# Performance work log

Hardware: AMD Instinct MI355X
Metric: run time of the kernel (lower is better)

The kernel has to match this reference:

```python
import jax, jax.numpy as jnp
import numpy as np

EPS = 1e-5

def _conv(x, w, stride=1, padding=0):
    return jax.lax.conv_general_dilated(
        x, w, window_strides=(stride, stride),
        padding=((padding, padding), (padding, padding)),
        dimension_numbers=('NCHW', 'OIHW', 'NCHW'))

def _bn(x, gamma, beta, mean, var):
    # inference-mode batchnorm, per-channel over NCHW
    inv = gamma / jnp.sqrt(var + EPS)
    return x * inv[None, :, None, None] + (beta - mean * inv)[None, :, None, None]

def setup_inputs() -> dict:
    key = jax.random.key(0)
    ks = jax.random.split(key, 16)
    B, Cin, H, W = 64, 1024, 28, 28
    width, Cout = 256, 1024
    d = {}
    d['x'] = jax.random.normal(ks[0], (B, Cin, H, W), jnp.float32)
    d['w1'] = jax.random.normal(ks[1], (width, Cin, 1, 1), jnp.float32) * 0.03
    d['w2'] = jax.random.normal(ks[2], (width, width, 3, 3), jnp.float32) * 0.02
    d['w3'] = jax.random.normal(ks[3], (Cout, width, 1, 1), jnp.float32) * 0.03
    for i, c in [(1, width), (2, width), (3, Cout)]:
        d[f'g{i}'] = jnp.ones((c,), jnp.float32)
        d[f'b{i}'] = jnp.zeros((c,), jnp.float32)
        d[f'm{i}'] = jax.random.normal(ks[4 + i], (c,), jnp.float32) * 0.1
        d[f'v{i}'] = jax.random.uniform(ks[8 + i], (c,), jnp.float32, 0.5, 1.5)
    return d

def reference(x, w1, w2, w3, g1, b1, m1, v1, g2, b2, m2, v2, g3, b3, m3, v3):
    out = jax.nn.relu(_bn(_conv(x, w1), g1, b1, m1, v1))
    out = jax.nn.relu(_bn(_conv(out, w2, stride=1, padding=1), g2, b2, m2, v2))
    out = _bn(_conv(out, w3), g3, b3, m3, v3)
    return jax.nn.relu(out + x)
```

## Files before the change

kernel.cpp:

```cpp
#include <hip/hip_runtime.h>
#include <hip/hip_bf16.h>
#include <cstdint>
#include <cstddef>

#define EPS_BN 1e-5f
#define LDK1 40
#define TILE1 (128 * LDK1)

typedef __attribute__((ext_vector_type(8))) __bf16 bf16x8;
typedef __attribute__((ext_vector_type(4))) float f32x4;

__device__ __forceinline__ unsigned short f2b(float f) {
    __hip_bfloat16 h = __float2bfloat16(f);
    return __builtin_bit_cast(unsigned short, h);
}
__device__ __forceinline__ unsigned int pack2(float a, float b) {
    return (unsigned int)f2b(a) | ((unsigned int)f2b(b) << 16);
}
__device__ __forceinline__ void lgkm_barrier() {
    __builtin_amdgcn_s_waitcnt(0xC07F);
    __builtin_amdgcn_s_barrier();
}


__global__ void prep_bn_kernel(const float* __restrict__ g1, const float* __restrict__ b1,
                               const float* __restrict__ m1, const float* __restrict__ v1,
                               const float* __restrict__ g2, const float* __restrict__ b2,
                               const float* __restrict__ m2, const float* __restrict__ v2,
                               const float* __restrict__ g3, const float* __restrict__ b3,
                               const float* __restrict__ m3, const float* __restrict__ v3,
                               float* __restrict__ bias1, float* __restrict__ bias2,
                               float* __restrict__ bias3) {
    int t = blockIdx.x * 256 + threadIdx.x;
    if (t < 256) {
        float inv = g1[t] * rsqrtf(v1[t] + EPS_BN);
        bias1[t] = b1[t] - m1[t] * inv;
    } else if (t < 512) {
        int c = t - 256;
        float inv = g2[c] * rsqrtf(v2[c] + EPS_BN);
        bias2[c] = b2[c] - m2[c] * inv;
    } else if (t < 1536) {
        int c = t - 512;
        float inv = g3[c] * rsqrtf(v3[c] + EPS_BN);
        bias3[c] = b3[c] - m3[c] * inv;
    }
}

__global__ void repack_w1(const float* __restrict__ w1, const float* __restrict__ g1,
                          const float* __restrict__ v1, unsigned short* __restrict__ w1b) {
    int idx = blockIdx.x * 256 + threadIdx.x;
    int co = idx >> 10;
    float inv = g1[co] * rsqrtf(v1[co] + EPS_BN);
    w1b[idx] = f2b(w1[idx] * inv);
}

__global__ void repack_w2(const float* __restrict__ w2, const float* __restrict__ g2,
                          const float* __restrict__ v2, unsigned short* __restrict__ w2r) {
    int idx = blockIdx.x * 256 + threadIdx.x;
    int k9 = idx >> 16;
    int rem = idx & 65535;
    int co = rem >> 8;
    int ci = rem & 255;
    float inv = g2[co] * rsqrtf(v2[co] + EPS_BN);
    w2r[idx] = f2b(w2[(co * 256 + ci) * 9 + k9] * inv);
}

__global__ void repack_w3(const float* __restrict__ w3, const float* __restrict__ g3,
                          const float* __restrict__ v3, unsigned short* __restrict__ w3b) {
    int idx = blockIdx.x * 256 + threadIdx.x;
    int co = idx >> 8;
    float inv = g3[co] * rsqrtf(v3[co] + EPS_BN);
    w3b[idx] = f2b(w3[idx] * inv);
}

__global__ void halo_zero(unsigned short* __restrict__ in2p) {
    int idx = blockIdx.x * 256 + threadIdx.x;
    int cell = idx >> 5, l8 = idx & 31;
    int n = cell / 116, c = cell % 116;
    int h, w;
    if (c < 30)      { h = 0;      w = c; }
    else if (c < 60) { h = 29;     w = c - 30; }
    else if (c < 88) { h = c - 59; w = 0; }
    else             { h = c - 87; w = 29; }
    uint4 z = {0u, 0u, 0u, 0u};
    *reinterpret_cast<uint4*>(in2p + (((size_t)n * 900) + h * 30 + w) * 256 + l8 * 8) = z;
}

__device__ __forceinline__ void mfma_step(const unsigned short* As, const unsigned short* Bs,
                                          int aoff, int boff, int ld, f32x4 acc[4][4]) {
    bf16x8 a[4], b[4];
#pragma unroll
    for (int i = 0; i < 4; ++i)
        a[i] = *reinterpret_cast<const bf16x8*>(As + aoff + i * 16 * ld);
#pragma unroll
    for (int j = 0; j < 4; ++j)
        b[j] = *reinterpret_cast<const bf16x8*>(Bs + boff + j * 16 * ld);
#pragma unroll
    for (int i = 0; i < 4; ++i)
#pragma unroll
        for (int j = 0; j < 4; ++j)
            acc[i][j] = __builtin_amdgcn_mfma_f32_16x16x32_bf16(a[i], b[j], acc[i][j], 0, 0, 0);
}

__global__ __launch_bounds__(512) void conv1_kernel(const float* __restrict__ x,
                                                    const unsigned short* __restrict__ w1b,
                                                    const float* __restrict__ bias1,
                                                    unsigned short* __restrict__ in2p) {
    __shared__ unsigned short As[2][256 * LDK1];
    __shared__ unsigned short Bs[2][128 * LDK1];
    const int tid = threadIdx.x;
    const int f0 = blockIdx.x * 128;
    const int lane = tid & 63, wave = tid >> 6;
    const int wA = wave & 3;
    const int wB = wave >> 2;
    const int l15 = lane & 15, quad = lane >> 4;

    const int ar = tid >> 1, ah = (tid & 1) * 16;
    const unsigned short* aptr = w1b + (size_t)ar * 1024 + ah;
    const int awo = ar * LDK1 + ah;

    const int cp = tid >> 5, sq = tid & 31;
    const float* xb[4];
    int bwo[4];
#pragma unroll
    for (int e = 0; e < 4; ++e) {
        int f = f0 + sq + 32 * e;
        int n = f / 784, sp = f - n * 784;
        xb[e] = x + ((size_t)n * 1024 + 2 * cp) * 784 + sp;
        bwo[e] = (sq + 32 * e) * LDK1 + 2 * cp;
    }

    f32x4 acc[4][4] = {};
    const int aoff = (wA * 64 + l15) * LDK1 + quad * 8;
    const int boff = (wB * 64 + l15) * LDK1 + quad * 8;

    uint4 ra0, ra1;
    float bv0[4], bv1[4];
    ra0 = *reinterpret_cast<const uint4*>(aptr);
    ra1 = *reinterpret_cast<const uint4*>(aptr + 8);
#pragma unroll
    for (int e = 0; e < 4; ++e) { bv0[e] = xb[e][0]; bv1[e] = xb[e][784]; }

    for (int kk = 0; kk < 32; ++kk) {
        unsigned short* A = As[kk & 1];
        unsigned short* B = Bs[kk & 1];
        *reinterpret_cast<uint4*>(A + awo) = ra0;
        *reinterpret_cast<uint4*>(A + awo + 8) = ra1;
#pragma unroll
        for (int e = 0; e < 4; ++e)
            *reinterpret_cast<unsigned int*>(B + bwo[e]) = pack2(bv0[e], bv1[e]);
        if (kk < 31) {
            int ka = (kk + 1) * 32;
            ra0 = *reinterpret_cast<const uint4*>(aptr + ka);
            ra1 = *reinterpret_cast<const uint4*>(aptr + ka + 8);
            size_t kb = (size_t)(kk + 1) * 32 * 784;
#pragma unroll
            for (int e = 0; e < 4; ++e) { bv0[e] = xb[e][kb]; bv1[e] = xb[e][kb + 784]; }
        }
        lgkm_barrier();
        mfma_step(A, B, aoff, boff, LDK1, acc);
    }

#pragma unroll
    for (int j = 0; j < 4; ++j) {
        int f = f0 + wB * 64 + j * 16 + l15;
        int n = f / 784;
        int r = f - n * 784;
        int oh = r / 28, ow = r - oh * 28;
        unsigned short* dst = in2p + ((size_t)n * 900 + (oh + 1) * 30 + (ow + 1)) * 256;
#pragma unroll
        for (int i = 0; i < 4; ++i) {
            int co = wA * 64 + i * 16 + quad * 4;
            float4 bia = *reinterpret_cast<const float4*>(bias1 + co);
            f32x4 v = acc[i][j];
            ushort4 o;
            o.x = f2b(fmaxf(v.x + bia.x, 0.f));
            o.y = f2b(fmaxf(v.y + bia.y, 0.f));
            o.z = f2b(fmaxf(v.z + bia.z, 0.f));
            o.w = f2b(fmaxf(v.w + bia.w, 0.f));
            *reinterpret_cast<ushort4*>(dst + co) = o;
        }
    }
}

__global__ __launch_bounds__(256) void conv2_kernel(const unsigned short* __restrict__ in2p,
                                                    const unsigned short* __restrict__ w2r,
                                                    const float* __restrict__ bias2,
                                                    unsigned short* __restrict__ in3) {
    __shared__ unsigned short As[2][TILE1];
    __shared__ unsigned short Bs[2][TILE1];
    const int tid = threadIdx.x;
    const int f0 = blockIdx.x * 128;
    const int m0 = blockIdx.y * 128;
    const int lane = tid & 63, wave = tid >> 6;
    const int wr = wave >> 1, wc = wave & 1;
    const int l15 = lane & 15, quad = lane >> 4;
    const int tcid = tid & 3, tcl = tid >> 2;

    int cellc[2];
#pragma unroll
    for (int p = 0; p < 2; ++p) {
        int f = f0 + p * 64 + tcl;
        int n = f / 784;
        int r = f - n * 784;
        int oh = r / 28, ow = r - oh * 28;
        cellc[p] = n * 900 + (oh + 1) * 30 + (ow + 1);
    }

    f32x4 acc[4][4] = {};
    const int aoff = (wr * 64 + l15) * LDK1 + quad * 8;
    const int boff = (wc * 64 + l15) * LDK1 + quad * 8;
    const int wo = tcl * LDK1 + tcid * 8;

    uint4 a0s0, a1s0, b0s0, b1s0, a0s1, a1s1, b0s1, b1s1;
    {
        a0s0 = *reinterpret_cast<const uint4*>(w2r + (size_t)(m0 + tcl) * 256 + tcid * 8);
        a1s0 = *reinterpret_cast<const uint4*>(w2r + (size_t)(m0 + 64 + tcl) * 256 + tcid * 8);
        b0s0 = *reinterpret_cast<const uint4*>(in2p + (size_t)(cellc[0] - 31) * 256 + tcid * 8);
        b1s0 = *reinterpret_cast<const uint4*>(in2p + (size_t)(cellc[1] - 31) * 256 + tcid * 8);
    }
    {
        const unsigned short* wb = w2r + 32;
        a0s1 = *reinterpret_cast<const uint4*>(wb + (size_t)(m0 + tcl) * 256 + tcid * 8);
        a1s1 = *reinterpret_cast<const uint4*>(wb + (size_t)(m0 + 64 + tcl) * 256 + tcid * 8);
        const unsigned short* bb = in2p + 32 + tcid * 8;
        b0s1 = *reinterpret_cast<const uint4*>(bb + (size_t)(cellc[0] - 31) * 256);
        b1s1 = *reinterpret_cast<const uint4*>(bb + (size_t)(cellc[1] - 31) * 256);
    }

    for (int kk = 0; kk < 72; kk += 2) {
        {
            unsigned short* A = As[0];
            unsigned short* B = Bs[0];
            *reinterpret_cast<uint4*>(A + wo) = a0s0;
            *reinterpret_cast<uint4*>(A + 64 * LDK1 + wo) = a1s0;
            *reinterpret_cast<uint4*>(B + wo) = b0s0;
            *reinterpret_cast<uint4*>(B + 64 * LDK1 + wo) = b1s0;
            if (kk < 70) {
                int kn = kk + 2;
                int k9 = kn >> 3, cb = kn & 7;
                int kh = k9 / 3, kw = k9 - 3 * kh;
                int dd = (kh - 1) * 30 + (kw - 1);
                const unsigned short* wb = w2r + (size_t)k9 * 65536 + cb * 32;
                a0s0 = *reinterpret_cast<const uint4*>(wb + (size_t)(m0 + tcl) * 256 + tcid * 8);
                a1s0 = *reinterpret_cast<const uint4*>(wb + (size_t)(m0 + 64 + tcl) * 256 + tcid * 8);
                const unsigned short* bb = in2p + (size_t)cb * 32 + tcid * 8;
                b0s0 = *reinterpret_cast<const uint4*>(bb + (size_t)(cellc[0] + dd) * 256);
                b1s0 = *reinterpret_cast<const uint4*>(bb + (size_t)(cellc[1] + dd) * 256);
            }
            lgkm_barrier();
            mfma_step(A, B, aoff, boff, LDK1, acc);
        }
        {
            unsigned short* A = As[1];
            unsigned short* B = Bs[1];
            *reinterpret_cast<uint4*>(A + wo) = a0s1;
            *reinterpret_cast<uint4*>(A + 64 * LDK1 + wo) = a1s1;
            *reinterpret_cast<uint4*>(B + wo) = b0s1;
            *reinterpret_cast<uint4*>(B + 64 * LDK1 + wo) = b1s1;
            if (kk < 70) {
                int kn = kk + 3;
                int k9 = kn >> 3, cb = kn & 7;
                int kh = k9 / 3, kw = k9 - 3 * kh;
                int dd = (kh - 1) * 30 + (kw - 1);
                const unsigned short* wb = w2r + (size_t)k9 * 65536 + cb * 32;
                a0s1 = *reinterpret_cast<const uint4*>(wb + (size_t)(m0 + tcl) * 256 + tcid * 8);
                a1s1 = *reinterpret_cast<const uint4*>(wb + (size_t)(m0 + 64 + tcl) * 256 + tcid * 8);
                const unsigned short* bb = in2p + (size_t)cb * 32 + tcid * 8;
                b0s1 = *reinterpret_cast<const uint4*>(bb + (size_t)(cellc[0] + dd) * 256);
                b1s1 = *reinterpret_cast<const uint4*>(bb + (size_t)(cellc[1] + dd) * 256);
            }
            lgkm_barrier();
            mfma_step(A, B, aoff, boff, LDK1, acc);
        }
    }

#pragma unroll
    for (int j = 0; j < 4; ++j) {
        int f = f0 + wc * 64 + j * 16 + l15;
        unsigned short* dst = in3 + (size_t)f * 256;
#pragma unroll
        for (int i = 0; i < 4; ++i) {
            int co = m0 + wr * 64 + i * 16 + quad * 4;
            float4 bia = *reinterpret_cast<const float4*>(bias2 + co);
            f32x4 v = acc[i][j];
            ushort4 o;
            o.x = f2b(fmaxf(v.x + bia.x, 0.f));
            o.y = f2b(fmaxf(v.y + bia.y, 0.f));
            o.z = f2b(fmaxf(v.z + bia.z, 0.f));
            o.w = f2b(fmaxf(v.w + bia.w, 0.f));
            *reinterpret_cast<ushort4*>(dst + co) = o;
        }
    }
}

__global__ __launch_bounds__(256) void conv3_kernel(const unsigned short* __restrict__ in3,
                                                    const unsigned short* __restrict__ w3b,
                                                    const float* __restrict__ bias3,
                                                    const float* __restrict__ x,
                                                    float* __restrict__ out) {
    __shared__ unsigned short As[2][TILE1];
    __shared__ unsigned short Bs[2][TILE1];
    const int tid = threadIdx.x;
    const int f0 = blockIdx.x * 128;
    const int m0 = blockIdx.y * 128;
    const int lane = tid & 63, wave = tid >> 6;
    const int wr = wave >> 1, wc = wave & 1;
    const int l15 = lane & 15, quad = lane >> 4;
    const int tcid = tid & 3, tcl = tid >> 2;

    const unsigned short* aptr = in3 + (size_t)(f0 + tcl) * 256 + tcid * 8;
    const unsigned short* bptr = w3b + (size_t)(m0 + tcl) * 256 + tcid * 8;

    const int aoff = (wr * 64 + l15) * LDK1 + quad * 8;
    const int boff = (wc * 64 + l15) * LDK1 + quad * 8;
    const int wo = tcl * LDK1 + tcid * 8;

    uint4 ra0, ra1, rb0, rb1;
    ra0 = *reinterpret_cast<const uint4*>(aptr);
    ra1 = *reinterpret_cast<const uint4*>(aptr + 16384);
    rb0 = *reinterpret_cast<const uint4*>(bptr);
    rb1 = *reinterpret_cast<const uint4*>(bptr + 16384);

    f32x4 acc[4][4];
#pragma unroll
    for (int j = 0; j < 4; ++j) {
        int co = m0 + wc * 64 + j * 16 + l15;
        float b = bias3[co];
#pragma unroll
        for (int i = 0; i < 4; ++i) {
            int fb = f0 + wr * 64 + i * 16 + quad * 4;
            int n = fb / 784;
            int sp = fb - n * 784;
            float4 xr = *reinterpret_cast<const float4*>(x + ((size_t)n * 1024 + co) * 784 + sp);
            f32x4 a;
            a.x = xr.x + b;
            a.y = xr.y + b;
            a.z = xr.z + b;
            a.w = xr.w + b;
            acc[i][j] = a;
        }
    }

    for (int kk = 0; kk < 8; ++kk) {
        unsigned short* A = As[kk & 1];
        unsigned short* B = Bs[kk & 1];
        *reinterpret_cast<uint4*>(A + wo) = ra0;
        *reinterpret_cast<uint4*>(A + 64 * LDK1 + wo) = ra1;
        *reinterpret_cast<uint4*>(B + wo) = rb0;
        *reinterpret_cast<uint4*>(B + 64 * LDK1 + wo) = rb1;
        if (kk < 7) {
            int k0 = (kk + 1) * 32;
            ra0 = *reinterpret_cast<const uint4*>(aptr + k0);
            ra1 = *reinterpret_cast<const uint4*>(aptr + 16384 + k0);
            rb0 = *reinterpret_cast<const uint4*>(bptr + k0);
            rb1 = *reinterpret_cast<const uint4*>(bptr + 16384 + k0);
        }
        lgkm_barrier();
        mfma_step(A, B, aoff, boff, LDK1, acc);
    }

#pragma unroll
    for (int j = 0; j < 4; ++j) {
        int co = m0 + wc * 64 + j * 16 + l15;
#pragma unroll
        for (int i = 0; i < 4; ++i) {
            int fb = f0 + wr * 64 + i * 16 + quad * 4;
            int n = fb / 784;
            int sp = fb - n * 784;
            size_t off = ((size_t)n * 1024 + co) * 784 + sp;
            f32x4 v = acc[i][j];
            float4 o;
            o.x = fmaxf(v.x, 0.f);
            o.y = fmaxf(v.y, 0.f);
            o.z = fmaxf(v.z, 0.f);
            o.w = fmaxf(v.w, 0.f);
            *reinterpret_cast<float4*>(out + off) = o;
        }
    }
}


extern "C" void kernel_launch(void* const* d_in, const int* in_sizes, int n_in,
                              void* d_out, int out_size, void* d_ws, size_t ws_size,
                              hipStream_t stream) {
    const float* x  = (const float*)d_in[0];
    const float* w1 = (const float*)d_in[1];
    const float* w2 = (const float*)d_in[2];
    const float* w3 = (const float*)d_in[3];
    const float* g1 = (const float*)d_in[4];
    const float* b1 = (const float*)d_in[5];
    const float* m1 = (const float*)d_in[6];
    const float* v1 = (const float*)d_in[7];
    const float* g2 = (const float*)d_in[8];
    const float* b2 = (const float*)d_in[9];
    const float* m2 = (const float*)d_in[10];
    const float* v2 = (const float*)d_in[11];
    const float* g3 = (const float*)d_in[12];
    const float* b3 = (const float*)d_in[13];
    const float* m3 = (const float*)d_in[14];
    const float* v3 = (const float*)d_in[15];

    char* ws = (char*)d_ws;
    unsigned short* w1b  = (unsigned short*)(ws + 0);
    unsigned short* w2r  = (unsigned short*)(ws + 524288);
    unsigned short* w3b  = (unsigned short*)(ws + 1703936);
    float* bias1         = (float*)(ws + 2228224);
    float* bias2         = (float*)(ws + 2229248);
    float* bias3         = (float*)(ws + 2230272);
    unsigned short* in2p = (unsigned short*)(ws + 2234368);
    unsigned short* in3  = (unsigned short*)(ws + 31725568);

    prep_bn_kernel<<<6, 256, 0, stream>>>(g1, b1, m1, v1, g2, b2, m2, v2, g3, b3, m3, v3,
                                          bias1, bias2, bias3);
    repack_w1<<<1024, 256, 0, stream>>>(w1, g1, v1, w1b);
    repack_w2<<<2304, 256, 0, stream>>>(w2, g2, v2, w2r);
    repack_w3<<<1024, 256, 0, stream>>>(w3, g3, v3, w3b);
    halo_zero<<<928, 256, 0, stream>>>(in2p);

    conv1_kernel<<<dim3(392), 512, 0, stream>>>(x, w1b, bias1, in2p);
    conv2_kernel<<<dim3(392, 2), 256, 0, stream>>>(in2p, w2r, bias2, in3);
    conv3_kernel<<<dim3(392, 8), 256, 0, stream>>>(in3, w3b, bias3, x, (float*)d_out);
}
```

Baseline: 591.7 us.

## Fuse 3x3 conv2 and 1x1 conv3 into one kernel via LDS staging

Replaces the separate conv2 and conv3 kernels with a single kernel in which each block computes all 256 conv2 output channels for 64 pixels. The result is kept in LDS as bf16 and then multiplied against w3 to produce all 1024 output channels with the residual and ReLU applied. This removes the global write and re-read of the intermediate activation and one kernel launch. In exchange, each block now reloads the full w2 slice with a smaller pixel tile, so weight traffic per output goes up, and the conv3 stage reads w3 straight from global memory without LDS staging.

Measured after the change: 692.6 us. +17.0%, slower.

```diff
diff --git a/kernel.cpp b/kernel.cpp
--- a/kernel.cpp
+++ b/kernel.cpp
@@ -5,7 +5,7 @@
 
 #define EPS_BN 1e-5f
 #define LDK1 40
-#define TILE1 (128 * LDK1)
+#define LDP 264
 
 typedef __attribute__((ext_vector_type(8))) __bf16 bf16x8;
 typedef __attribute__((ext_vector_type(4))) float f32x4;
@@ -183,199 +183,146 @@
     }
 }
 
-__global__ __launch_bounds__(256) void conv2_kernel(const unsigned short* __restrict__ in2p,
-                                                    const unsigned short* __restrict__ w2r,
-                                                    const float* __restrict__ bias2,
-                                                    unsigned short* __restrict__ in3) {
-    __shared__ unsigned short As[2][TILE1];
-    __shared__ unsigned short Bs[2][TILE1];
+__global__ __launch_bounds__(256) void conv23_kernel(const unsigned short* __restrict__ in2p,
+                                                     const unsigned short* __restrict__ w2r,
+                                                     const float* __restrict__ bias2,
+                                                     const unsigned short* __restrict__ w3b,
+                                                     const float* __restrict__ bias3,
+                                                     const float* __restrict__ x,
+                                                     float* __restrict__ out) {
+    __shared__ unsigned short lds[25600];
+    unsigned short* A2w = lds;
+    unsigned short* B2f = lds + 20480;
+    unsigned short* P   = lds;
+
     const int tid = threadIdx.x;
-    const int f0 = blockIdx.x * 128;
-    const int m0 = blockIdx.y * 128;
-    const int lane = tid & 63, wave = tid >> 6;
-    const int wr = wave >> 1, wc = wave & 1;
+    const int F0 = blockIdx.x * 64;
+    const int lane = tid & 63, wv = tid >> 6;
     const int l15 = lane & 15, quad = lane >> 4;
-    const int tcid = tid & 3, tcl = tid >> 2;
-
-    int cellc[2];
-#pragma unroll
-    for (int p = 0; p < 2; ++p) {
-        int f = f0 + p * 64 + tcl;
+    const int trow = tid >> 2, tc8 = (tid & 3) * 8;
+
+    int cellc;
+    {
+        int f = F0 + trow;
         int n = f / 784;
         int r = f - n * 784;
         int oh = r / 28, ow = r - oh * 28;
-        cellc[p] = n * 900 + (oh + 1) * 30 + (ow + 1);
-    }
+        cellc = n * 900 + (oh + 1) * 30 + (ow + 1);
+    }
+    const unsigned short* wbase = w2r + (size_t)trow * 256 + tc8;
 
     f32x4 acc[4][4] = {};
-    const int aoff = (wr * 64 + l15) * LDK1 + quad * 8;
-    const int boff = (wc * 64 + l15) * LDK1 + quad * 8;
-    const int wo = tcl * LDK1 + tcid * 8;
-
-    uint4 a0s0, a1s0, b0s0, b1s0, a0s1, a1s1, b0s1, b1s1;
+    const int aoffA = (wv * 64 + l15) * LDK1 + quad * 8;
+    const int boffB = l15 * LDK1 + quad * 8;
+    const int woA = trow * LDK1 + tc8;
+    const int woB = trow * LDK1 + tc8;
+
+    uint4 rW0, rW1, rW2, rW3, rS;
     {
-        a0s0 = *reinterpret_cast<const uint4*>(w2r + (size_t)(m0 + tcl) * 256 + tcid * 8);
-        a1s0 = *reinterpret_cast<const uint4*>(w2r + (size_t)(m0 + 64 + tcl) * 256 + tcid * 8);
-        b0s0 = *reinterpret_cast<const uint4*>(in2p + (size_t)(cellc[0] - 31) * 256 + tcid * 8);
-        b1s0 = *reinterpret_cast<const uint4*>(in2p + (size_t)(cellc[1] - 31) * 256 + tcid * 8);
-    }
-    {
-        const unsigned short* wb = w2r + 32;
-        a0s1 = *reinterpret_cast<const uint4*>(wb + (size_t)(m0 + tcl) * 256 + tcid * 8);
-        a1s1 = *reinterpret_cast<const uint4*>(wb + (size_t)(m0 + 64 + tcl) * 256 + tcid * 8);
-        const unsigned short* bb = in2p + 32 + tcid * 8;
-        b0s1 = *reinterpret_cast<const uint4*>(bb + (size_t)(cellc[0] - 31) * 256);
-        b1s1 = *reinterpret_cast<const uint4*>(bb + (size_t)(cellc[1] - 31) * 256);
-    }
-
-    for (int kk = 0; kk < 72; kk += 2) {
-        {
-            unsigned short* A = As[0];
-            unsigned short* B = Bs[0];
-            *reinterpret_cast<uint4*>(A + wo) = a0s0;
-            *reinterpret_cast<uint4*>(A + 64 * LDK1 + wo) = a1s0;
-            *reinterpret_cast<uint4*>(B + wo) = b0s0;
-            *reinterpret_cast<uint4*>(B + 64 * LDK1 + wo) = b1s0;
-            if (kk < 70) {
-                int kn = kk + 2;
-                int k9 = kn >> 3, cb = kn & 7;
-                int kh = k9 / 3, kw = k9 - 3 * kh;
-                int dd = (kh - 1) * 30 + (kw - 1);
-                const unsigned short* wb = w2r + (size_t)k9 * 65536 + cb * 32;
-                a0s0 = *reinterpret_cast<const uint4*>(wb + (size_t)(m0 + tcl) * 256 + tcid * 8);
-                a1s0 = *reinterpret_cast<const uint4*>(wb + (size_t)(m0 + 64 + tcl) * 256 + tcid * 8);
-                const unsigned short* bb = in2p + (size_t)cb * 32 + tcid * 8;
-                b0s0 = *reinterpret_cast<const uint4*>(bb + (size_t)(cellc[0] + dd) * 256);
-                b1s0 = *reinterpret_cast<const uint4*>(bb + (size_t)(cellc[1] + dd) * 256);
+        rW0 = *reinterpret_cast<const uint4*>(wbase);
+        rW1 = *reinterpret_cast<const uint4*>(wbase + 64 * 256);
+        rW2 = *reinterpret_cast<const uint4*>(wbase + 128 * 256);
+        rW3 = *reinterpret_cast<const uint4*>(wbase + 192 * 256);
+        rS  = *reinterpret_cast<const uint4*>(in2p + (size_t)(cellc - 31) * 256 + tc8);
+    }
+    for (int kk = 0; kk < 72; ++kk) {
+        unsigned short* Aw = A2w + (kk & 1) * 10240;
+        unsigned short* Bf = B2f + (kk & 1) * 2560;
+        *reinterpret_cast<uint4*>(Aw + woA) = rW0;
+        *reinterpret_cast<uint4*>(Aw + woA + 64 * LDK1) = rW1;
+        *reinterpret_cast<uint4*>(Aw + woA + 128 * LDK1) = rW2;
+        *reinterpret_cast<uint4*>(Aw + woA + 192 * LDK1) = rW3;
+        *reinterpret_cast<uint4*>(Bf + woB) = rS;
+        if (kk < 71) {
+            int kn = kk + 1;
+            int k9 = kn >> 3, cb = kn & 7;
+            int kh = k9 / 3, kw = k9 - 3 * kh;
+            int dd = (kh - 1) * 30 + (kw - 1);
+            const unsigned short* wb = w2r + (size_t)k9 * 65536 + cb * 32 + (size_t)trow * 256 + tc8;
+            rW0 = *reinterpret_cast<const uint4*>(wb);
+            rW1 = *reinterpret_cast<const uint4*>(wb + 64 * 256);
+            rW2 = *reinterpret_cast<const uint4*>(wb + 128 * 256);
+            rW3 = *reinterpret_cast<const uint4*>(wb + 192 * 256);
+            rS  = *reinterpret_cast<const uint4*>(in2p + (size_t)(cellc + dd) * 256 + cb * 32 + tc8);
+        }
+        lgkm_barrier();
+        mfma_step(Aw, Bf, aoffA, boffB, LDK1, acc);
+    }
+
+    __syncthreads();
+#pragma unroll
+    for (int j = 0; j < 4; ++j) {
+        int fcol = j * 16 + l15;
+#pragma unroll
+        for (int i = 0; i < 4; ++i) {
+            int co2b = wv * 64 + i * 16 + quad * 4;
+            float4 bia = *reinterpret_cast<const float4*>(bias2 + co2b);
+            f32x4 v = acc[i][j];
+            ushort4 pk;
+            pk.x = f2b(fmaxf(v.x + bia.x, 0.f));
+            pk.y = f2b(fmaxf(v.y + bia.y, 0.f));
+            pk.z = f2b(fmaxf(v.z + bia.z, 0.f));
+            pk.w = f2b(fmaxf(v.w + bia.w, 0.f));
+            *reinterpret_cast<ushort4*>(P + fcol * LDP + co2b) = pk;
+        }
+    }
+    lgkm_barrier();
+
+    const int aoff3 = l15 * LDP + quad * 8;
+    for (int t3 = 0; t3 < 4; ++t3) {
+        int n0 = t3 * 256;
+#pragma unroll
+        for (int j = 0; j < 4; ++j) {
+            int co3 = n0 + wv * 64 + j * 16 + l15;
+            float b3 = bias3[co3];
+#pragma unroll
+            for (int i = 0; i < 4; ++i) {
+                int fb = F0 + i * 16 + quad * 4;
+                int n = fb / 784;
+                int sp = fb - n * 784;
+                float4 xr = *reinterpret_cast<const float4*>(x + ((size_t)n * 1024 + co3) * 784 + sp);
+                f32x4 a;
+                a.x = xr.x + b3;
+                a.y = xr.y + b3;
+                a.z = xr.z + b3;
+                a.w = xr.w + b3;
+                acc[i][j] = a;
             }
-            lgkm_barrier();
-            mfma_step(A, B, aoff, boff, LDK1, acc);
-        }
-        {
-            unsigned short* A = As[1];
-            unsigned short* B = Bs[1];
-            *reinterpret_cast<uint4*>(A + wo) = a0s1;
-            *reinterpret_cast<uint4*>(A + 64 * LDK1 + wo) = a1s1;
-            *reinterpret_cast<uint4*>(B + wo) = b0s1;
-            *reinterpret_cast<uint4*>(B + 64 * LDK1 + wo) = b1s1;
-            if (kk < 70) {
-                int kn = kk + 3;
-                int k9 = kn >> 3, cb = kn & 7;
-                int kh = k9 / 3, kw = k9 - 3 * kh;
-                int dd = (kh - 1) * 30 + (kw - 1);
-                const unsigned short* wb = w2r + (size_t)k9 * 65536 + cb * 32;
-                a0s1 = *reinterpret_cast<const uint4*>(wb + (size_t)(m0 + tcl) * 256 + tcid * 8);
-                a1s1 = *reinterpret_cast<const uint4*>(wb + (size_t)(m0 + 64 + tcl) * 256 + tcid * 8);
-                const unsigned short* bb = in2p + (size_t)cb * 32 + tcid * 8;
-                b0s1 = *reinterpret_cast<const uint4*>(bb + (size_t)(cellc[0] + dd) * 256);
-                b1s1 = *reinterpret_cast<const uint4*>(bb + (size_t)(cellc[1] + dd) * 256);
+        }
+#pragma unroll
+        for (int kk = 0; kk < 8; ++kk) {
+            bf16x8 a[4], b[4];
+#pragma unroll
+            for (int i = 0; i < 4; ++i)
+                a[i] = *reinterpret_cast<const bf16x8*>(P + aoff3 + i * 16 * LDP + kk * 32);
+#pragma unroll
+            for (int j = 0; j < 4; ++j) {
+                size_t co3r = (size_t)(n0 + wv * 64 + j * 16 + l15);
+                b[j] = *reinterpret_cast<const bf16x8*>(w3b + co3r * 256 + kk * 32 + quad * 8);
             }
-            lgkm_barrier();
-            mfma_step(A, B, aoff, boff, LDK1, acc);
-        }
-    }
-
-#pragma unroll
-    for (int j = 0; j < 4; ++j) {
-        int f = f0 + wc * 64 + j * 16 + l15;
-        unsigned short* dst = in3 + (size_t)f * 256;
-#pragma unroll
-        for (int i = 0; i < 4; ++i) {
-            int co = m0 + wr * 64 + i * 16 + quad * 4;
-            float4 bia = *reinterpret_cast<const float4*>(bias2 + co);
-            f32x4 v = acc[i][j];
-            ushort4 o;
-            o.x = f2b(fmaxf(v.x + bia.x, 0.f));
-            o.y = f2b(fmaxf(v.y + bia.y, 0.f));
-            o.z = f2b(fmaxf(v.z + bia.z, 0.f));
-            o.w = f2b(fmaxf(v.w + bia.w, 0.f));
-            *reinterpret_cast<ushort4*>(dst + co) = o;
-        }
-    }
-}
-
-__global__ __launch_bounds__(256) void conv3_kernel(const unsigned short* __restrict__ in3,
-                                                    const unsigned short* __restrict__ w3b,
-                                                    const float* __restrict__ bias3,
-                                                    const float* __restrict__ x,
-                                                    float* __restrict__ out) {
-    __shared__ unsigned short As[2][TILE1];
-    __shared__ unsigned short Bs[2][TILE1];
-    const int tid = threadIdx.x;
-    const int f0 = blockIdx.x * 128;
-    const int m0 = blockIdx.y * 128;
-    const int lane = tid & 63, wave = tid >> 6;
-    const int wr = wave >> 1, wc = wave & 1;
-    const int l15 = lane & 15, quad = lane >> 4;
-    const int tcid = tid & 3, tcl = tid >> 2;
-
-    const unsigned short* aptr = in3 + (size_t)(f0 + tcl) * 256 + tcid * 8;
-    const unsigned short* bptr = w3b + (size_t)(m0 + tcl) * 256 + tcid * 8;
-
-    const int aoff = (wr * 64 + l15) * LDK1 + quad * 8;
-    const int boff = (wc * 64 + l15) * LDK1 + quad * 8;
-    const int wo = tcl * LDK1 + tcid * 8;
-
-    uint4 ra0, ra1, rb0, rb1;
-    ra0 = *reinterpret_cast<const uint4*>(aptr);
-    ra1 = *reinterpret_cast<const uint4*>(aptr + 16384);
-    rb0 = *reinterpret_cast<const uint4*>(bptr);
-    rb1 = *reinterpret_cast<const uint4*>(bptr + 16384);
-
-    f32x4 acc[4][4];
-#pragma unroll
-    for (int j = 0; j < 4; ++j) {
-        int co = m0 + wc * 64 + j * 16 + l15;
-        float b = bias3[co];
-#pragma unroll
-        for (int i = 0; i < 4; ++i) {
-            int fb = f0 + wr * 64 + i * 16 + quad * 4;
-            int n = fb / 784;
-            int sp = fb - n * 784;
-            float4 xr = *reinterpret_cast<const float4*>(x + ((size_t)n * 1024 + co) * 784 + sp);
-            f32x4 a;
-            a.x = xr.x + b;
-            a.y = xr.y + b;
-            a.z = xr.z + b;
-            a.w = xr.w + b;
-            acc[i][j] = a;
-        }
-    }
-
-    for (int kk = 0; kk < 8; ++kk) {
-        unsigned short* A = As[kk & 1];
-        unsigned short* B = Bs[kk & 1];
-        *reinterpret_cast<uint4*>(A + wo) = ra0;
-        *reinterpret_cast<uint4*>(A + 64 * LDK1 + wo) = ra1;
-        *reinterpret_cast<uint4*>(B + wo) = rb0;
-        *reinterpret_cast<uint4*>(B + 64 * LDK1 + wo) = rb1;
-        if (kk < 7) {
-            int k0 = (kk + 1) * 32;
-            ra0 = *reinterpret_cast<const uint4*>(aptr + k0);
-            ra1 = *reinterpret_cast<const uint4*>(aptr + 16384 + k0);
-            rb0 = *reinterpret_cast<const uint4*>(bptr + k0);
-            rb1 = *reinterpret_cast<const uint4*>(bptr + 16384 + k0);
-        }
-        lgkm_barrier();
-        mfma_step(A, B, aoff, boff, LDK1, acc);
-    }
-
-#pragma unroll
-    for (int j = 0; j < 4; ++j) {
-        int co = m0 + wc * 64 + j * 16 + l15;
-#pragma unroll
-        for (int i = 0; i < 4; ++i) {
-            int fb = f0 + wr * 64 + i * 16 + quad * 4;
-            int n = fb / 784;
-            int sp = fb - n * 784;
-            size_t off = ((size_t)n * 1024 + co) * 784 + sp;
-            f32x4 v = acc[i][j];
-            float4 o;
-            o.x = fmaxf(v.x, 0.f);
-            o.y = fmaxf(v.y, 0.f);
-            o.z = fmaxf(v.z, 0.f);
-            o.w = fmaxf(v.w, 0.f);
-            *reinterpret_cast<float4*>(out + off) = o;
+#pragma unroll
+            for (int i = 0; i < 4; ++i)
+#pragma unroll
+                for (int j = 0; j < 4; ++j)
+                    acc[i][j] = __builtin_amdgcn_mfma_f32_16x16x32_bf16(a[i], b[j], acc[i][j], 0, 0, 0);
+        }
+#pragma unroll
+        for (int j = 0; j < 4; ++j) {
+            int co3 = n0 + wv * 64 + j * 16 + l15;
+#pragma unroll
+            for (int i = 0; i < 4; ++i) {
+                int fb = F0 + i * 16 + quad * 4;
+                int n = fb / 784;
+                int sp = fb - n * 784;
+                size_t off = ((size_t)n * 1024 + co3) * 784 + sp;
+                f32x4 v = acc[i][j];
+                float4 o;
+                o.x = fmaxf(v.x, 0.f);
+                o.y = fmaxf(v.y, 0.f);
+                o.z = fmaxf(v.z, 0.f);
+                o.w = fmaxf(v.w, 0.f);
+                *reinterpret_cast<float4*>(out + off) = o;
+            }
         }
     }
 }
@@ -409,7 +356,6 @@
     float* bias2         = (float*)(ws + 2229248);
     float* bias3         = (float*)(ws + 2230272);
     unsigned short* in2p = (unsigned short*)(ws + 2234368);
-    unsigned short* in3  = (unsigned short*)(ws + 31725568);
 
     prep_bn_kernel<<<6, 256, 0, stream>>>(g1, b1, m1, v1, g2, b2, m2, v2, g3, b3, m3, v3,
                                           bias1, bias2, bias3);
@@ -419,6 +365,6 @@
     halo_zero<<<928, 256, 0, stream>>>(in2p);
 
     conv1_kernel<<<dim3(392), 512, 0, stream>>>(x, w1b, bias1, in2p);
-    conv2_kernel<<<dim3(392, 2), 256, 0, stream>>>(in2p, w2r, bias2, in3);
-    conv3_kernel<<<dim3(392, 8), 256, 0, stream>>>(in3, w3b, bias3, x, (float*)d_out);
-}
+    conv23_kernel<<<dim3(784), 256, 0, stream>>>(in2p, w2r, bias2, w3b, bias3, x,
+                                                 (float*)d_out);
+}
```
